# Kernel tuning notes

Hardware: AMD Instinct MI355X
Metric: run time of the kernel (lower is better)

## Reference

```python
import jax, jax.numpy as jnp
import numpy as np

EPS = 1e-6
N_HEADS, N_POINTS = 6, 4


def layer_norm(x, w, b):
    m = jnp.mean(x, -1, keepdims=True)
    v = jnp.mean((x - m) ** 2, -1, keepdims=True)
    return (x - m) * jax.lax.rsqrt(v + EPS) * w + b


def bilinear_sample(val, loc, Hl, Wl):
    # val: (B, nH, Hl*Wl, d); loc: (B, Lq, nH, P, 2) in [0,1]
    # matches F.grid_sample(mode='bilinear', padding='zeros', align_corners=False)
    B, nH, _, d = val.shape
    Lq, P = loc.shape[1], loc.shape[3]
    x = loc[..., 0] * Wl - 0.5
    y = loc[..., 1] * Hl - 0.5
    x0 = jnp.floor(x)
    y0 = jnp.floor(y)
    wx1 = x - x0
    wy1 = y - y0
    out = jnp.zeros((B, nH, Lq * P, d), val.dtype)
    corners = ((0, 0, (1 - wy1) * (1 - wx1)), (0, 1, (1 - wy1) * wx1),
               (1, 0, wy1 * (1 - wx1)), (1, 1, wy1 * wx1))
    for dy, dx, w in corners:
        xi = x0 + dx
        yi = y0 + dy
        valid = (xi >= 0) & (xi < Wl) & (yi >= 0) & (yi < Hl)
        xi_c = jnp.clip(xi, 0, Wl - 1).astype(jnp.int32)
        yi_c = jnp.clip(yi, 0, Hl - 1).astype(jnp.int32)
        idx = (yi_c * Wl + xi_c).transpose(0, 2, 1, 3).reshape(B, nH, Lq * P)
        g = jnp.take_along_axis(val, idx[..., None], axis=2)  # (B,nH,Lq*P,d)
        ww = jnp.where(valid, w, 0.0).transpose(0, 2, 1, 3).reshape(B, nH, Lq * P)
        out = out + g * ww[..., None]
    return out.reshape(B, nH, Lq, P, d).transpose(0, 2, 1, 3, 4)  # (B,Lq,nH,P,d)


def dwconv3x3(x, w, b):
    # x: (N, C, H, W); w: (C, 1, 3, 3) depthwise
    y = jax.lax.conv_general_dilated(x, w, (1, 1), 'SAME',
                                     feature_group_count=w.shape[0],
                                     dimension_numbers=('NCHW', 'OIHW', 'NCHW'))
    return y + b[None, :, None, None]


def setup_inputs() -> dict:
    key = jax.random.key(0)
    ks = jax.random.split(key, 16)
    B, H, W, C = 8, 32, 32, 768
    Lq = 3 * H * W
    Hf = Wf = 64
    hidden = int(C * 0.25)
    s = 0.02
    inp = {
        'query': jax.random.normal(ks[0], (B, Lq, C), jnp.float32),
        'reference_points': jax.random.uniform(ks[1], (B, Lq, 1, 2), jnp.float32),
        'feat': jax.random.normal(ks[2], (B, Hf * Wf, C), jnp.float32),
        'spatial_shapes': jnp.array([[Hf, Wf]], jnp.int32),
        'level_start_index': jnp.zeros((1,), jnp.int32),
        'H': H, 'W': W,
        'qn_w': jnp.ones((C,)), 'qn_b': jnp.zeros((C,)),
        'fn_w': jnp.ones((C,)), 'fn_b': jnp.zeros((C,)),
        'so_w': jax.random.normal(ks[3], (C, N_HEADS * N_POINTS * 2)) * s,
        'so_b': jax.random.normal(ks[4], (N_HEADS * N_POINTS * 2,)) * s,
        'aw_w': jax.random.normal(ks[5], (C, N_HEADS * N_POINTS)) * s,
        'aw_b': jnp.zeros((N_HEADS * N_POINTS,)),
        'vp_w': jax.random.normal(ks[6], (C, C)) * s,
        'vp_b': jnp.zeros((C,)),
        'op_w': jax.random.normal(ks[7], (C, C)) * s,
        'op_b': jnp.zeros((C,)),
        'ffn_w': jnp.ones((C,)), 'ffn_b': jnp.zeros((C,)),
        'fc1_w': jax.random.normal(ks[8], (C, hidden)) * s,
        'fc1_b': jnp.zeros((hidden,)),
        'dw_w': jax.random.normal(ks[9], (hidden, 1, 3, 3)) * s,
        'dw_b': jnp.zeros((hidden,)),
        'fc2_w': jax.random.normal(ks[10], (hidden, C)) * s,
        'fc2_b': jnp.zeros((C,)),
    }
    return inp


def reference(query, reference_points, feat, spatial_shapes, level_start_index, H, W,
              qn_w, qn_b, fn_w, fn_b, so_w, so_b, aw_w, aw_b, vp_w, vp_b, op_w, op_b,
              ffn_w, ffn_b, fc1_w, fc1_b, dw_w, dw_b, fc2_w, fc2_b):
    B, Lq, C = query.shape
    nH, nP = N_HEADS, N_POINTS
    d = C // nH
    ss = np.asarray(spatial_shapes)
    Hl, Wl = int(ss[0, 0]), int(ss[0, 1])

    # --- MSDeformAttn (single level) ---
    q = layer_norm(query, qn_w, qn_b)
    f = layer_norm(feat, fn_w, fn_b)
    value = (f @ vp_w + vp_b).reshape(B, Hl * Wl, nH, d).transpose(0, 2, 1, 3)  # (B,nH,Lin,d)
    offs = (q @ so_w + so_b).reshape(B, Lq, nH, 1, nP, 2)
    aw = jax.nn.softmax((q @ aw_w + aw_b).reshape(B, Lq, nH, nP), axis=-1)
    normalizer = jnp.array([Wl, Hl], query.dtype)
    loc = reference_points[:, :, None, :, None, :] + offs / normalizer  # (B,Lq,nH,1,nP,2)
    sampled = bilinear_sample(value, loc[:, :, :, 0], Hl, Wl)           # (B,Lq,nH,nP,d)
    attn = (sampled * aw[..., None]).sum(3).reshape(B, Lq, C) @ op_w + op_b
    query = query + attn

    # --- ConvFFN (3 equal HxW chunks through shared depthwise conv) ---
    x = layer_norm(query, ffn_w, ffn_b) @ fc1_w + fc1_b  # (B, 3*H*W, hid)
    n = Lq // 3
    hid = fc1_w.shape[1]
    xc = x.reshape(B, 3, n, hid).transpose(0, 1, 3, 2).reshape(B * 3, hid, H, W)
    xc = dwconv3x3(xc, dw_w, dw_b)
    x = xc.reshape(B, 3, hid, n).transpose(0, 1, 3, 2).reshape(B, Lq, hid)
    x = jax.nn.gelu(x, approximate=False)
    x = x @ fc2_w + fc2_b
    return query + x
```

## Files before the change

### kernel.cpp

```cpp
#include <hip/hip_runtime.h>
#include <hip/hip_bf16.h>
#include <math.h>

typedef __hip_bfloat16 bf16;
typedef short bf16x8 __attribute__((ext_vector_type(8)));
typedef short bf16x4 __attribute__((ext_vector_type(4)));
typedef float f32x4 __attribute__((ext_vector_type(4)));

#define NB 8
#define LQ 3072
#define CC 768
#define NHEADS 6
#define NPTS 4
#define DHEAD 128
#define HLVL 64
#define WLVL 64
#define LIN 4096
#define HID 192
#define BLTOT 24576
#define FROWS 32768

__device__ __forceinline__ float bf2f(short u)
{ return __uint_as_float(((unsigned)(unsigned short)u) << 16); }

template<int N_>
__device__ __forceinline__ void wait_vmcnt()
{
    if constexpr (N_ == 0)      asm volatile("s_waitcnt vmcnt(0)" ::: "memory");
    else if constexpr (N_ == 2) asm volatile("s_waitcnt vmcnt(2)" ::: "memory");
    else if constexpr (N_ == 4) asm volatile("s_waitcnt vmcnt(4)" ::: "memory");
    else if constexpr (N_ == 6) asm volatile("s_waitcnt vmcnt(6)" ::: "memory");
    else if constexpr (N_ == 8) asm volatile("s_waitcnt vmcnt(8)" ::: "memory");
    else static_assert(N_ == 0, "add a vmcnt case");
}

__global__ __launch_bounds__(256)
void ln_f32_wave_kernel(const float* __restrict__ x, const float* __restrict__ w,
                        const float* __restrict__ b, bf16* __restrict__ out)
{
    const int row = blockIdx.x * 4 + (threadIdx.x >> 6);
    const int lane = threadIdx.x & 63;
    const f32x4* xr = (const f32x4*)(x + (size_t)row * CC);
    f32x4 f0 = xr[lane], f1 = xr[64 + lane], f2 = xr[128 + lane];
    float s = 0.f, ss = 0.f;
    #pragma unroll
    for (int k = 0; k < 4; ++k) {
        s += f0[k] + f1[k] + f2[k];
        ss += f0[k] * f0[k] + f1[k] * f1[k] + f2[k] * f2[k];
    }
    #pragma unroll
    for (int o = 32; o > 0; o >>= 1) { s += __shfl_down(s, o); ss += __shfl_down(ss, o); }
    s = __shfl(s, 0); ss = __shfl(ss, 0);
    const float m = s * (1.f / CC);
    const float rs = rsqrtf(ss * (1.f / CC) - m * m + 1e-6f);
    const f32x4* w4 = (const f32x4*)w;
    const f32x4* b4 = (const f32x4*)b;
    bf16* orow = out + (size_t)row * CC;
    #pragma unroll
    for (int j = 0; j < 3; ++j) {
        f32x4 fj = (j == 0) ? f0 : (j == 1) ? f1 : f2;
        f32x4 wj = w4[j * 64 + lane], bj = b4[j * 64 + lane];
        bf16 t4[4];
        #pragma unroll
        for (int k = 0; k < 4; ++k) t4[k] = __float2bfloat16((fj[k] - m) * rs * wj[k] + bj[k]);
        *(bf16x4*)(orow + j * 256 + lane * 4) = *(bf16x4*)t4;
    }
}

__global__ __launch_bounds__(256)
void wt_bf16_kernel(const float* __restrict__ src, bf16* __restrict__ dst, int K, int N)
{
    __shared__ float t[64][65];
    const int tn0 = blockIdx.x * 64, tk0 = blockIdx.y * 64;
    const int r = threadIdx.x >> 6, c = threadIdx.x & 63;
    #pragma unroll
    for (int i = 0; i < 16; ++i) {
        const int k = i * 4 + r;
        t[k][c] = src[(size_t)(tk0 + k) * N + tn0 + c];
    }
    __syncthreads();
    #pragma unroll
    for (int i = 0; i < 16; ++i) {
        const int n = i * 4 + r;
        dst[(size_t)(tn0 + n) * K + tk0 + c] = __float2bfloat16(t[c][n]);
    }
}

__global__ __launch_bounds__(256)
void build_dots_w(const float* __restrict__ so_w, const float* __restrict__ so_b,
                  const float* __restrict__ aw_w, const float* __restrict__ aw_b,
                  bf16* __restrict__ wt, float* __restrict__ db)
{
    int i = blockIdx.x * 256 + threadIdx.x;
    if (i < 128 * 768) {
        int n = i / 768, k = i - n * 768;
        float v = 0.f;
        if (n < 48) v = so_w[(size_t)k * 48 + n];
        else if (n < 72) v = aw_w[(size_t)k * 24 + (n - 48)];
        wt[i] = __float2bfloat16(v);
    }
    if (i < 128) {
        float bv = 0.f;
        if (i < 48) bv = so_b[i];
        else if (i < 72) bv = aw_b[i - 48];
        db[i] = bv;
    }
}

template<int BM, int BN, int WM, int WN, int MODE>
__global__ __launch_bounds__(256)
void gemm_kernel(const bf16* __restrict__ A, const bf16* __restrict__ Bt,
                 const float* __restrict__ bias, const void* __restrict__ resv,
                 void* __restrict__ outv, int M, int N, int K)
{
    constexpr int WAVES_N = BN / WN;
    constexpr int FM = WM / 16, FN = WN / 16;
    constexpr int CWA = BM / 32;
    constexpr int CWB = BN / 32;
    constexpr int LPT = CWA + CWB;
    constexpr int ABYTES = BM * 256;
    constexpr int DBUF_BYTES = (BM + BN) * 256;
    constexpr int EPI_BYTES = BM * BN * 4;
    constexpr size_t SMEM_BYTES = DBUF_BYTES > EPI_BYTES ? DBUF_BYTES : EPI_BYTES;
    __shared__ __align__(16) char smem[SMEM_BYTES];
    bf16* sA = (bf16*)smem;
    bf16* sB = (bf16*)(smem + ABYTES);
    float* epi = (float*)smem;

    const int tid = threadIdx.x;
    const int lane = tid & 63;
    const int wave = tid >> 6;

    const int nwgx = gridDim.x;
    const int nwg = nwgx * gridDim.y;
    const int bid = blockIdx.y * nwgx + blockIdx.x;
    const int swz = (bid & 7) * (nwg >> 3) + (bid >> 3);
    const int m0 = (swz / nwgx) * BM;
    const int n0 = (swz % nwgx) * BN;

    const int wm = (wave / WAVES_N) * WM;
    const int wn = (wave % WAVES_N) * WN;

    const int srow = lane >> 3;
    const int scol = ((lane & 7) ^ srow) * 8;

    constexpr int GPR8 = BN / 8;
    constexpr int GPT8 = (BM * BN / 8) / 256;
    constexpr int QPR4 = BN / 4;
    constexpr int QPT4 = (BM * BN / 4) / 256;
    float4 pr0[GPT8], pr1[GPT8];
    bf16x4 prb[QPT4];
    if constexpr (MODE == 3) {
        const float* resf = (const float*)resv;
        #pragma unroll
        for (int k = 0; k < GPT8; ++k) {
            const int f = k * 256 + tid;
            const int rr = f / GPR8, cc = (f % GPR8) * 8;
            const size_t gidx = (size_t)(m0 + rr) * N + n0 + cc;
            pr0[k] = *(const float4*)&resf[gidx];
            pr1[k] = *(const float4*)&resf[gidx + 4];
        }
    }
    if constexpr (MODE == 4) {
        const bf16* resb = (const bf16*)resv;
        #pragma unroll
        for (int k = 0; k < QPT4; ++k) {
            const int f = k * 256 + tid;
            const int rr = f / QPR4, cc = (f % QPR4) * 4;
            prb[k] = *(const bf16x4*)&resb[(size_t)(m0 + rr) * N + n0 + cc];
        }
    }

#define STAGE(tt, half)                                                                            \
    { const int k0_ = (tt) * 64;                                                                   \
      _Pragma("unroll")                                                                            \
      for (int i_ = 0; i_ < CWA; ++i_) {                                                           \
        const int c_ = i_ * 4 + wave;                                                              \
        __builtin_amdgcn_global_load_lds(                                                          \
          (const __attribute__((address_space(1))) void*)(A + (size_t)(m0 + c_ * 8 + srow) * K + k0_ + scol), \
          (__attribute__((address_space(3))) void*)(sA + (half) * (BM * 64) + c_ * 512), 16, 0, 0); } \
      _Pragma("unroll")                                                                            \
      for (int i_ = 0; i_ < CWB; ++i_) {                                                           \
        const int c_ = i_ * 4 + wave;                                                              \
        __builtin_amdgcn_global_load_lds(                                                          \
          (const __attribute__((address_space(1))) void*)(Bt + (size_t)(n0 + c_ * 8 + srow) * K + k0_ + scol), \
          (__attribute__((address_space(3))) void*)(sB + (half) * (BN * 64) + c_ * 512), 16, 0, 0); } }

    f32x4 acc[FM][FN] = {};
    const int nt = K >> 6;

    STAGE(0, 0);
    STAGE(1, 1);

    for (int t = 0; t < nt; ++t) {
        const int half = t & 1;
        if (t + 1 < nt) wait_vmcnt<LPT>();
        else            wait_vmcnt<0>();
        __builtin_amdgcn_s_barrier();
        const bf16* cA = sA + half * (BM * 64);
        const bf16* cB = sB + half * (BN * 64);
        #pragma unroll
        for (int kki = 0; kki < 2; ++kki) {
            const int kslot = kki * 4 + (lane >> 4);
            bf16x8 aF[FM], bF[FN];
            #pragma unroll
            for (int i = 0; i < FM; ++i) {
                const int row = wm + i * 16 + (lane & 15);
                aF[i] = *(const bf16x8*)(&cA[row * 64 + ((kslot ^ (row & 7)) * 8)]);
            }
            #pragma unroll
            for (int j = 0; j < FN; ++j) {
                const int row = wn + j * 16 + (lane & 15);
                bF[j] = *(const bf16x8*)(&cB[row * 64 + ((kslot ^ (row & 7)) * 8)]);
            }
            #pragma unroll
            for (int i = 0; i < FM; ++i) {
                #pragma unroll
                for (int j = 0; j < FN; ++j)
                    acc[i][j] = __builtin_amdgcn_mfma_f32_16x16x32_bf16(aF[i], bF[j], acc[i][j], 0, 0, 0);
            }
        }
        asm volatile("s_waitcnt lgkmcnt(0)" ::: "memory");
        __builtin_amdgcn_s_barrier();
        if (t + 2 < nt) STAGE(t + 2, half);
    }
#undef STAGE

    #pragma unroll
    for (int j = 0; j < FN; ++j) {
        const int colL = wn + j * 16 + (lane & 15);
        const float bj = bias[n0 + colL];
        #pragma unroll
        for (int i = 0; i < FM; ++i) {
            #pragma unroll
            for (int r = 0; r < 4; ++r) {
                const int rowL = wm + i * 16 + ((lane >> 4) << 2) + r;
                const int addr = rowL * BN + ((((colL >> 2) ^ (rowL & 7)) << 2) | (colL & 3));
                epi[addr] = acc[i][j][r] + bj;
            }
        }
    }
    __syncthreads();

    if constexpr (MODE == 0 || MODE == 3) {
        #pragma unroll
        for (int k = 0; k < GPT8; ++k) {
            const int f = k * 256 + tid;
            const int rr = f / GPR8, cc = (f % GPR8) * 8;
            const int g0 = ((cc >> 2) ^ (rr & 7)) << 2;
            const int g1 = (((cc >> 2) + 1) ^ (rr & 7)) << 2;
            float4 v0 = *(const float4*)&epi[rr * BN + g0];
            float4 v1 = *(const float4*)&epi[rr * BN + g1];
            if constexpr (MODE == 3) {
                v0.x += pr0[k].x; v0.y += pr0[k].y; v0.z += pr0[k].z; v0.w += pr0[k].w;
                v1.x += pr1[k].x; v1.y += pr1[k].y; v1.z += pr1[k].z; v1.w += pr1[k].w;
            }
            bf16 tmp[8];
            tmp[0] = __float2bfloat16(v0.x); tmp[1] = __float2bfloat16(v0.y);
            tmp[2] = __float2bfloat16(v0.z); tmp[3] = __float2bfloat16(v0.w);
            tmp[4] = __float2bfloat16(v1.x); tmp[5] = __float2bfloat16(v1.y);
            tmp[6] = __float2bfloat16(v1.z); tmp[7] = __float2bfloat16(v1.w);
            *(bf16x8*)((bf16*)outv + (size_t)(m0 + rr) * N + n0 + cc) = *(bf16x8*)tmp;
        }
    } else {
        #pragma unroll
        for (int k = 0; k < QPT4; ++k) {
            const int f = k * 256 + tid;
            const int rr = f / QPR4, cc = (f % QPR4) * 4;
            const int gs = ((cc >> 2) ^ (rr & 7)) << 2;
            float4 v = *(const float4*)&epi[rr * BN + gs];
            if constexpr (MODE == 4) {
                v.x += bf2f(prb[k][0]); v.y += bf2f(prb[k][1]);
                v.z += bf2f(prb[k][2]); v.w += bf2f(prb[k][3]);
            }
            *(float4*)&((float*)outv)[(size_t)(m0 + rr) * N + n0 + cc] = v;
        }
    }
}

template<int BM, int BN, int WM, int WN, bool F32IN, int EPI>
__global__ __launch_bounds__(256)
void ln_gemm_kernel(const void* __restrict__ xv, const float* __restrict__ lnw,
                    const float* __restrict__ lnb, const bf16* __restrict__ Bt,
                    const float* __restrict__ bias, const float* __restrict__ refp,
                    void* __restrict__ outv, int M, int N)
{
    constexpr int WAVES_N = BN / WN;
    constexpr int FM = WM / 16, FN = WN / 16;
    constexpr int CWB = BN / 32;
    constexpr int RPW = BM / 4;
    static_assert(BM * BN * 4 <= 2 * BN * 64 * 2, "epi must fit in sB");
    __shared__ __align__(16) bf16 sA[BM * 768];
    __shared__ __align__(16) char sBmem[2 * BN * 64 * 2];
    bf16* sB = (bf16*)sBmem;
    float* epi = (float*)sBmem;

    const int tid = threadIdx.x;
    const int lane = tid & 63;
    const int wave = tid >> 6;

    const int nwgx = gridDim.x;
    const int nwg = nwgx * gridDim.y;
    const int bid = blockIdx.y * nwgx + blockIdx.x;
    const int swz = (bid & 7) * (nwg >> 3) + (bid >> 3);
    const int m0 = (swz / nwgx) * BM;
    const int n0 = (swz % nwgx) * BN;

    const int wm = (wave / WAVES_N) * WM;
    const int wn = (wave % WAVES_N) * WN;
    const int srow = lane >> 3;
    const int scol = ((lane & 7) ^ srow) * 8;

#define STAGEB(tt, half)                                                                           \
    { const int k0_ = (tt) * 64;                                                                   \
      _Pragma("unroll")                                                                            \
      for (int i_ = 0; i_ < CWB; ++i_) {                                                           \
        const int c_ = i_ * 4 + wave;                                                              \
        __builtin_amdgcn_global_load_lds(                                                          \
          (const __attribute__((address_space(1))) void*)(Bt + (size_t)(n0 + c_ * 8 + srow) * 768 + k0_ + scol), \
          (__attribute__((address_space(3))) void*)(sB + (half) * (BN * 64) + c_ * 512), 16, 0, 0); } }

    STAGEB(0, 0);
    STAGEB(1, 1);

    if constexpr (F32IN) {
        const f32x4* w4 = (const f32x4*)lnw;
        const f32x4* b4 = (const f32x4*)lnb;
        f32x4 wv0 = w4[lane], wv1 = w4[64 + lane], wv2 = w4[128 + lane];
        f32x4 bv0 = b4[lane], bv1 = b4[64 + lane], bv2 = b4[128 + lane];
        for (int rr = 0; rr < RPW; ++rr) {
            const int r = wave * RPW + rr;
            const f32x4* xr = (const f32x4*)((const float*)xv + (size_t)(m0 + r) * 768);
            f32x4 f0 = xr[lane], f1 = xr[64 + lane], f2 = xr[128 + lane];
            float s = 0.f, ss = 0.f;
            #pragma unroll
            for (int k = 0; k < 4; ++k) {
                s += f0[k] + f1[k] + f2[k];
                ss += f0[k] * f0[k] + f1[k] * f1[k] + f2[k] * f2[k];
            }
            #pragma unroll
            for (int o = 32; o > 0; o >>= 1) { s += __shfl_down(s, o); ss += __shfl_down(ss, o); }
            s = __shfl(s, 0); ss = __shfl(ss, 0);
            const float mn = s * (1.f / 768);
            const float rs = rsqrtf(ss * (1.f / 768) - mn * mn + 1e-6f);
            const int rx7 = r & 7;
            const int slot = (lane >> 1) & 7;
            const int off = (lane & 1) * 4;
            #pragma unroll
            for (int j = 0; j < 3; ++j) {
                f32x4 fj = (j == 0) ? f0 : (j == 1) ? f1 : f2;
                f32x4 wj = (j == 0) ? wv0 : (j == 1) ? wv1 : wv2;
                f32x4 bj = (j == 0) ? bv0 : (j == 1) ? bv1 : bv2;
                bf16 t4[4];
                #pragma unroll
                for (int k = 0; k < 4; ++k)
                    t4[k] = __float2bfloat16((fj[k] - mn) * rs * wj[k] + bj[k]);
                const int kt = j * 4 + (lane >> 4);
                *(bf16x4*)&sA[r * 768 + kt * 64 + ((slot ^ rx7) << 3) + off] = *(bf16x4*)t4;
            }
        }
    } else {
        const f32x4* w4 = (const f32x4*)lnw;
        const f32x4* b4 = (const f32x4*)lnb;
        f32x4 w80 = w4[lane * 2], w81 = w4[lane * 2 + 1], w44 = w4[128 + lane];
        f32x4 b80 = b4[lane * 2], b81 = b4[lane * 2 + 1], b44 = b4[128 + lane];
        for (int rr = 0; rr < RPW; ++rr) {
            const int r = wave * RPW + rr;
            const bf16* xr = (const bf16*)xv + (size_t)(m0 + r) * 768;
            bf16x8 v8 = *(const bf16x8*)(xr + lane * 8);
            bf16x4 v4 = *(const bf16x4*)(xr + 512 + lane * 4);
            float f[12];
            #pragma unroll
            for (int k = 0; k < 8; ++k) f[k] = bf2f(v8[k]);
            #pragma unroll
            for (int k = 0; k < 4; ++k) f[8 + k] = bf2f(v4[k]);
            float s = 0.f, ss = 0.f;
            #pragma unroll
            for (int k = 0; k < 12; ++k) { s += f[k]; ss += f[k] * f[k]; }
            #pragma unroll
            for (int o = 32; o > 0; o >>= 1) { s += __shfl_down(s, o); ss += __shfl_down(ss, o); }
            s = __shfl(s, 0); ss = __shfl(ss, 0);
            const float mn = s * (1.f / 768);
            const float rs = rsqrtf(ss * (1.f / 768) - mn * mn + 1e-6f);
            const int rx7 = r & 7;
            bf16 t8[8];
            #pragma unroll
            for (int k = 0; k < 4; ++k) t8[k] = __float2bfloat16((f[k] - mn) * rs * w80[k] + b80[k]);
            #pragma unroll
            for (int k = 0; k < 4; ++k) t8[4 + k] = __float2bfloat16((f[4 + k] - mn) * rs * w81[k] + b81[k]);
            *(bf16x8*)&sA[r * 768 + (lane >> 3) * 64 + (((lane & 7) ^ rx7) << 3)] = *(bf16x8*)t8;
            bf16 t4[4];
            #pragma unroll
            for (int k = 0; k < 4; ++k) t4[k] = __float2bfloat16((f[8 + k] - mn) * rs * w44[k] + b44[k]);
            *(bf16x4*)&sA[r * 768 + (8 + (lane >> 4)) * 64 + ((((lane >> 1) & 7) ^ rx7) << 3) + (lane & 1) * 4]
                = *(bf16x4*)t4;
        }
    }
    asm volatile("s_waitcnt lgkmcnt(0)" ::: "memory");

    f32x4 acc[FM][FN] = {};
    for (int t = 0; t < 12; ++t) {
        const int half = t & 1;
        if (t + 1 < 12) wait_vmcnt<CWB>();
        else            wait_vmcnt<0>();
        __builtin_amdgcn_s_barrier();
        const bf16* cB = sB + half * (BN * 64);
        #pragma unroll
        for (int kki = 0; kki < 2; ++kki) {
            const int kslot = kki * 4 + (lane >> 4);
            bf16x8 aF[FM], bF[FN];
            #pragma unroll
            for (int i = 0; i < FM; ++i) {
                const int row = wm + i * 16 + (lane & 15);
                aF[i] = *(const bf16x8*)(&sA[row * 768 + t * 64 + ((kslot ^ (row & 7)) * 8)]);
            }
            #pragma unroll
            for (int j = 0; j < FN; ++j) {
                const int row = wn + j * 16 + (lane & 15);
                bF[j] = *(const bf16x8*)(&cB[row * 64 + ((kslot ^ (row & 7)) * 8)]);
            }
            #pragma unroll
            for (int i = 0; i < FM; ++i) {
                #pragma unroll
                for (int j = 0; j < FN; ++j)
                    acc[i][j] = __builtin_amdgcn_mfma_f32_16x16x32_bf16(aF[i], bF[j], acc[i][j], 0, 0, 0);
            }
        }
        asm volatile("s_waitcnt lgkmcnt(0)" ::: "memory");
        __builtin_amdgcn_s_barrier();
        if (t + 2 < 12) STAGEB(t + 2, half);
    }
#undef STAGEB

    #pragma unroll
    for (int j = 0; j < FN; ++j) {
        const int colL = wn + j * 16 + (lane & 15);
        const float bj = bias[n0 + colL];
        #pragma unroll
        for (int i = 0; i < FM; ++i) {
            #pragma unroll
            for (int r = 0; r < 4; ++r) {
                const int rowL = wm + i * 16 + ((lane >> 4) << 2) + r;
                const int addr = rowL * BN + ((((colL >> 2) ^ (rowL & 7)) << 2) | (colL & 3));
                epi[addr] = acc[i][j][r] + bj;
            }
        }
    }
    __syncthreads();

    if constexpr (EPI == 1) {
        if (tid < BM * NHEADS) {
            const int rowL = tid & (BM - 1);
            const int h = tid / BM;
            auto erd = [&](int col) -> float {
                return epi[rowL * BN + ((((col >> 2) ^ (rowL & 7)) << 2) | (col & 3))];
            };
            float l0 = erd(48 + h * 4 + 0), l1 = erd(48 + h * 4 + 1);
            float l2 = erd(48 + h * 4 + 2), l3 = erd(48 + h * 4 + 3);
            float mx = fmaxf(fmaxf(l0, l1), fmaxf(l2, l3));
            float e0 = expf(l0 - mx), e1 = expf(l1 - mx), e2 = expf(l2 - mx), e3 = expf(l3 - mx);
            float inv = 1.f / (e0 + e1 + e2 + e3);
            float ee[4] = {e0, e1, e2, e3};
            const float rx = refp[(size_t)(m0 + rowL) * 2];
            const float ry = refp[(size_t)(m0 + rowL) * 2 + 1];
            float4* pp = (float4*)outv + ((size_t)(m0 + rowL) * NHEADS + h) * 4;
            #pragma unroll
            for (int p = 0; p < 4; ++p) {
                float ox = erd(h * 8 + p * 2), oy = erd(h * 8 + p * 2 + 1);
                pp[p] = make_float4(rx + ox * (1.f / WLVL), ry + oy * (1.f / HLVL), ee[p] * inv, 0.f);
            }
        }
    } else {
        constexpr int GPR8 = BN / 8;
        constexpr int GPT8 = (BM * BN / 8) / 256;
        #pragma unroll
        for (int k = 0; k < GPT8; ++k) {
            const int f = k * 256 + tid;
            const int rr = f / GPR8, cc = (f % GPR8) * 8;
            const int g0 = ((cc >> 2) ^ (rr & 7)) << 2;
            const int g1 = (((cc >> 2) + 1) ^ (rr & 7)) << 2;
            float4 v0 = *(const float4*)&epi[rr * BN + g0];
            float4 v1 = *(const float4*)&epi[rr * BN + g1];
            bf16 tmp[8];
            tmp[0] = __float2bfloat16(v0.x); tmp[1] = __float2bfloat16(v0.y);
            tmp[2] = __float2bfloat16(v0.z); tmp[3] = __float2bfloat16(v0.w);
            tmp[4] = __float2bfloat16(v1.x); tmp[5] = __float2bfloat16(v1.y);
            tmp[6] = __float2bfloat16(v1.z); tmp[7] = __float2bfloat16(v1.w);
            *(bf16x8*)((bf16*)outv + (size_t)(m0 + rr) * N + n0 + cc) = *(bf16x8*)tmp;
        }
    }
}

__global__ __launch_bounds__(256)
void sampler_kernel(const bf16* __restrict__ value, const float4* __restrict__ params,
                    bf16* __restrict__ attn_in)
{
    const int tid = threadIdx.x;
    const int cpx = gridDim.x >> 3;
    const int gblk = (blockIdx.x & 7) * cpx + (blockIdx.x >> 3);
    const int g = gblk * 16 + (tid >> 4);
    const int lane16 = tid & 15;
    const int bl = g / NHEADS;
    const int h = g - bl * NHEADS;
    const int b = bl / LQ;
    const bf16* vh = value + (size_t)b * LIN * CC + h * DHEAD + lane16 * 8;

    int offs[16];
    float wgt[16];
    #pragma unroll
    for (int p = 0; p < NPTS; ++p) {
        float4 pr = params[(size_t)g * 4 + p];
        float x = pr.x * (float)WLVL - 0.5f;
        float y = pr.y * (float)HLVL - 0.5f;
        float x0f = floorf(x), y0f = floorf(y);
        float wx1 = x - x0f, wy1 = y - y0f;
        float wx0 = 1.f - wx1, wy0 = 1.f - wy1;
        int x0 = (int)x0f, y0 = (int)y0f;
        #pragma unroll
        for (int dy = 0; dy < 2; ++dy) {
            const int yi = y0 + dy;
            const int yc = min(max(yi, 0), HLVL - 1);
            const float wy = (dy ? wy1 : wy0) * ((yi >= 0 && yi < HLVL) ? pr.z : 0.f);
            #pragma unroll
            for (int dx = 0; dx < 2; ++dx) {
                const int xi = x0 + dx;
                const int xc = min(max(xi, 0), WLVL - 1);
                const int idx = p * 4 + dy * 2 + dx;
                offs[idx] = (yc * WLVL + xc) * CC;
                wgt[idx] = wy * (dx ? wx1 : wx0) * ((xi >= 0 && xi < WLVL) ? 1.f : 0.f);
            }
        }
    }
    bf16x8 v[16];
    #pragma unroll
    for (int i = 0; i < 16; ++i) v[i] = *(const bf16x8*)(vh + offs[i]);
    float acc[8] = {};
    #pragma unroll
    for (int i = 0; i < 16; ++i) {
        #pragma unroll
        for (int j = 0; j < 8; ++j)
            acc[j] += wgt[i] * bf2f(v[i][j]);
    }
    bf16 tmp[8];
    #pragma unroll
    for (int j = 0; j < 8; ++j) tmp[j] = __float2bfloat16(acc[j]);
    *(bf16x8*)(attn_in + (size_t)bl * CC + h * DHEAD + lane16 * 8) = *(bf16x8*)tmp;
}

__global__ __launch_bounds__(192)
void dwconv_gelu_kernel(const bf16* __restrict__ z, const float* __restrict__ dw_w,
                        const float* __restrict__ dw_b, bf16* __restrict__ g)
{
    const int tp = threadIdx.x / 48;
    const int tc = threadIdx.x % 48;
    const int m = blockIdx.x * 4 + tp;
    const int c = tc * 4;
    const int pix = m & 1023;
    const int h = pix >> 5, w = pix & 31;
    float acc[4];
    #pragma unroll
    for (int j = 0; j < 4; ++j) acc[j] = dw_b[c + j];
    #pragma unroll
    for (int dy = -1; dy <= 1; ++dy) {
        int hh2 = h + dy;
        if (hh2 < 0 || hh2 >= 32) continue;
        #pragma unroll
        for (int dx = -1; dx <= 1; ++dx) {
            int ww2 = w + dx;
            if (ww2 < 0 || ww2 >= 32) continue;
            bf16x4 vv = *(const bf16x4*)&z[(size_t)(m + dy * 32 + dx) * HID + c];
            #pragma unroll
            for (int j = 0; j < 4; ++j)
                acc[j] += bf2f(vv[j]) * dw_w[(c + j) * 9 + (dy + 1) * 3 + (dx + 1)];
        }
    }
    bf16 tmp[4];
    #pragma unroll
    for (int j = 0; j < 4; ++j) {
        float ge = acc[j] * 0.5f * (1.f + erff(acc[j] * 0.70710678118f));
        tmp[j] = __float2bfloat16(ge);
    }
    *(bf16x4*)&g[(size_t)m * HID + c] = *(bf16x4*)tmp;
}

extern "C" void kernel_launch(void* const* d_in, const int* in_sizes, int n_in,
                              void* d_out, int out_size, void* d_ws, size_t ws_size,
                              hipStream_t stream)
{
    const float* query = (const float*)d_in[0];
    const float* refp  = (const float*)d_in[1];
    const float* feat  = (const float*)d_in[2];
    const float* qn_w = (const float*)d_in[7];
    const float* qn_b = (const float*)d_in[8];
    const float* fn_w = (const float*)d_in[9];
    const float* fn_b = (const float*)d_in[10];
    const float* so_w = (const float*)d_in[11];
    const float* so_b = (const float*)d_in[12];
    const float* aw_w = (const float*)d_in[13];
    const float* aw_b = (const float*)d_in[14];
    const float* vp_w = (const float*)d_in[15];
    const float* vp_b = (const float*)d_in[16];
    const float* op_w = (const float*)d_in[17];
    const float* op_b = (const float*)d_in[18];
    const float* ffn_w = (const float*)d_in[19];
    const float* ffn_b = (const float*)d_in[20];
    const float* fc1_w = (const float*)d_in[21];
    const float* fc1_b = (const float*)d_in[22];
    const float* dw_w = (const float*)d_in[23];
    const float* dw_b = (const float*)d_in[24];
    const float* fc2_w = (const float*)d_in[25];
    const float* fc2_b = (const float*)d_in[26];
    float* out = (float*)d_out;

    if (ws_size < (size_t)125829632) return;
    char* ws = (char*)d_ws;
    bf16* vp_wt   = (bf16*)(ws + 0);
    bf16* op_wt   = (bf16*)(ws + 1179648);
    bf16* fc1_wt  = (bf16*)(ws + 2359296);
    bf16* fc2_wt  = (bf16*)(ws + 2654208);
    bf16* dots_wt = (bf16*)(ws + 2949120);
    float* dots_b = (float*)(ws + 3145728);
    char* paramsR = ws + 3146240;
    char* dotsR   = ws + 12583424;
    char* regA = ws + 25166336;
    char* regB = ws + 75497984;
    float4* params = (float4*)paramsR;
    bf16* g        = (bf16*)paramsR;
    bf16* z        = (bf16*)dotsR;
    bf16* f_ln    = (bf16*)regA;
    bf16* attn_in = (bf16*)regA;
    bf16* value = (bf16*)regB;
    bf16* s_bf  = (bf16*)regB;

    wt_bf16_kernel<<<dim3(12, 12), 256, 0, stream>>>(vp_w, vp_wt, 768, 768);
    wt_bf16_kernel<<<dim3(12, 12), 256, 0, stream>>>(op_w, op_wt, 768, 768);
    wt_bf16_kernel<<<dim3(3, 12), 256, 0, stream>>>(fc1_w, fc1_wt, 768, 192);
    wt_bf16_kernel<<<dim3(12, 3), 256, 0, stream>>>(fc2_w, fc2_wt, 192, 768);
    build_dots_w<<<384, 256, 0, stream>>>(so_w, so_b, aw_w, aw_b, dots_wt, dots_b);

    ln_gemm_kernel<32, 128, 16, 64, true, 1><<<dim3(1, BLTOT / 32), 256, 0, stream>>>(
        query, qn_w, qn_b, dots_wt, dots_b, refp, params, BLTOT, 128);
    ln_f32_wave_kernel<<<FROWS / 4, 256, 0, stream>>>(feat, fn_w, fn_b, f_ln);
    gemm_kernel<128, 128, 64, 64, 0><<<dim3(6, FROWS / 128), 256, 0, stream>>>(
        f_ln, vp_wt, vp_b, nullptr, value, FROWS, 768, 768);
    sampler_kernel<<<(BLTOT * NHEADS) / 16, 256, 0, stream>>>(value, params, attn_in);
    gemm_kernel<64, 128, 32, 64, 3><<<dim3(6, BLTOT / 64), 256, 0, stream>>>(
        attn_in, op_wt, op_b, query, s_bf, BLTOT, 768, 768);

    ln_gemm_kernel<32, 64, 32, 16, false, 0><<<dim3(3, BLTOT / 32), 256, 0, stream>>>(
        s_bf, ffn_w, ffn_b, fc1_wt, fc1_b, nullptr, z, BLTOT, HID);
    dwconv_gelu_kernel<<<BLTOT / 4, 192, 0, stream>>>(z, dw_w, dw_b, g);
    gemm_kernel<64, 128, 32, 64, 4><<<dim3(6, BLTOT / 64), 256, 0, stream>>>(
        g, fc2_wt, fc2_b, s_bf, out, BLTOT, 768, HID);
}
```

Baseline: 327.2 us.

## Triple-buffer GEMM K-tiles and merge weight-prep launches into one kernel

Both GEMM kernels move from double to triple buffering of the K-tile shared memory stages, issuing loads three tiles ahead with matching vmcnt waits, so global-to-LDS latency is hidden more deeply. The five small weight transpose/convert launches are merged into a single prep kernel dispatched by block index, removing per-launch overhead. The extra buffer raises LDS use per block, which may lower occupancy, especially in ln_gemm where sA is already large.

```diff
diff --git a/kernel.cpp b/kernel.cpp
--- a/kernel.cpp
+++ b/kernel.cpp
@@ -26,11 +26,13 @@
 template<int N_>
 __device__ __forceinline__ void wait_vmcnt()
 {
-    if constexpr (N_ == 0)      asm volatile("s_waitcnt vmcnt(0)" ::: "memory");
-    else if constexpr (N_ == 2) asm volatile("s_waitcnt vmcnt(2)" ::: "memory");
-    else if constexpr (N_ == 4) asm volatile("s_waitcnt vmcnt(4)" ::: "memory");
-    else if constexpr (N_ == 6) asm volatile("s_waitcnt vmcnt(6)" ::: "memory");
-    else if constexpr (N_ == 8) asm volatile("s_waitcnt vmcnt(8)" ::: "memory");
+    if constexpr (N_ == 0)       asm volatile("s_waitcnt vmcnt(0)" ::: "memory");
+    else if constexpr (N_ == 2)  asm volatile("s_waitcnt vmcnt(2)" ::: "memory");
+    else if constexpr (N_ == 4)  asm volatile("s_waitcnt vmcnt(4)" ::: "memory");
+    else if constexpr (N_ == 6)  asm volatile("s_waitcnt vmcnt(6)" ::: "memory");
+    else if constexpr (N_ == 8)  asm volatile("s_waitcnt vmcnt(8)" ::: "memory");
+    else if constexpr (N_ == 12) asm volatile("s_waitcnt vmcnt(12)" ::: "memory");
+    else if constexpr (N_ == 16) asm volatile("s_waitcnt vmcnt(16)" ::: "memory");
     else static_assert(N_ == 0, "add a vmcnt case");
 }
 
@@ -67,43 +69,50 @@
     }
 }
 
+__device__ __forceinline__ void wt_tile(float (*t)[65], const float* __restrict__ src,
+                                        bf16* __restrict__ dst, int K, int N, int tn0, int tk0)
+{
+    const int r = threadIdx.x >> 6, c = threadIdx.x & 63;
+    #pragma unroll
+    for (int i = 0; i < 16; ++i)
+        t[i * 4 + r][c] = src[(size_t)(tk0 + i * 4 + r) * N + tn0 + c];
+    __syncthreads();
+    #pragma unroll
+    for (int i = 0; i < 16; ++i)
+        dst[(size_t)(tn0 + i * 4 + r) * K + tk0 + c] = __float2bfloat16(t[c][i * 4 + r]);
+}
+
 __global__ __launch_bounds__(256)
-void wt_bf16_kernel(const float* __restrict__ src, bf16* __restrict__ dst, int K, int N)
+void prep_kernel(const float* __restrict__ vp_w, const float* __restrict__ op_w,
+                 const float* __restrict__ fc1_w, const float* __restrict__ fc2_w,
+                 const float* __restrict__ so_w, const float* __restrict__ so_b,
+                 const float* __restrict__ aw_w, const float* __restrict__ aw_b,
+                 bf16* __restrict__ vp_wt, bf16* __restrict__ op_wt,
+                 bf16* __restrict__ fc1_wt, bf16* __restrict__ fc2_wt,
+                 bf16* __restrict__ dots_wt, float* __restrict__ db)
 {
     __shared__ float t[64][65];
-    const int tn0 = blockIdx.x * 64, tk0 = blockIdx.y * 64;
-    const int r = threadIdx.x >> 6, c = threadIdx.x & 63;
-    #pragma unroll
-    for (int i = 0; i < 16; ++i) {
-        const int k = i * 4 + r;
-        t[k][c] = src[(size_t)(tk0 + k) * N + tn0 + c];
-    }
-    __syncthreads();
-    #pragma unroll
-    for (int i = 0; i < 16; ++i) {
-        const int n = i * 4 + r;
-        dst[(size_t)(tn0 + n) * K + tk0 + c] = __float2bfloat16(t[c][n]);
-    }
-}
-
-__global__ __launch_bounds__(256)
-void build_dots_w(const float* __restrict__ so_w, const float* __restrict__ so_b,
-                  const float* __restrict__ aw_w, const float* __restrict__ aw_b,
-                  bf16* __restrict__ wt, float* __restrict__ db)
-{
-    int i = blockIdx.x * 256 + threadIdx.x;
-    if (i < 128 * 768) {
-        int n = i / 768, k = i - n * 768;
-        float v = 0.f;
-        if (n < 48) v = so_w[(size_t)k * 48 + n];
-        else if (n < 72) v = aw_w[(size_t)k * 24 + (n - 48)];
-        wt[i] = __float2bfloat16(v);
-    }
-    if (i < 128) {
-        float bv = 0.f;
-        if (i < 48) bv = so_b[i];
-        else if (i < 72) bv = aw_b[i - 48];
-        db[i] = bv;
+    int b = blockIdx.x;
+    if (b < 144)      wt_tile(t, vp_w, vp_wt, 768, 768, (b % 12) * 64, (b / 12) * 64);
+    else if (b < 288) { b -= 144; wt_tile(t, op_w, op_wt, 768, 768, (b % 12) * 64, (b / 12) * 64); }
+    else if (b < 324) { b -= 288; wt_tile(t, fc1_w, fc1_wt, 768, 192, (b % 3) * 64, (b / 3) * 64); }
+    else if (b < 360) { b -= 324; wt_tile(t, fc2_w, fc2_wt, 192, 768, (b % 12) * 64, (b / 12) * 64); }
+    else {
+        b -= 360;
+        int i = b * 256 + threadIdx.x;
+        if (i < 128 * 768) {
+            int n = i / 768, k = i - n * 768;
+            float v = 0.f;
+            if (n < 48) v = so_w[(size_t)k * 48 + n];
+            else if (n < 72) v = aw_w[(size_t)k * 24 + (n - 48)];
+            dots_wt[i] = __float2bfloat16(v);
+        }
+        if (i < 128) {
+            float bv = 0.f;
+            if (i < 48) bv = so_b[i];
+            else if (i < 72) bv = aw_b[i - 48];
+            db[i] = bv;
+        }
     }
 }
 
@@ -118,8 +127,8 @@
     constexpr int CWA = BM / 32;
     constexpr int CWB = BN / 32;
     constexpr int LPT = CWA + CWB;
-    constexpr int ABYTES = BM * 256;
-    constexpr int DBUF_BYTES = (BM + BN) * 256;
+    constexpr int ABYTES = 3 * BM * 128;
+    constexpr int DBUF_BYTES = 3 * (BM + BN) * 128;
     constexpr int EPI_BYTES = BM * BN * 4;
     constexpr size_t SMEM_BYTES = DBUF_BYTES > EPI_BYTES ? DBUF_BYTES : EPI_BYTES;
     __shared__ __align__(16) char smem[SMEM_BYTES];
@@ -171,34 +180,36 @@
         }
     }
 
-#define STAGE(tt, half)                                                                            \
+#define STAGE(tt, buf)                                                                             \
     { const int k0_ = (tt) * 64;                                                                   \
       _Pragma("unroll")                                                                            \
       for (int i_ = 0; i_ < CWA; ++i_) {                                                           \
         const int c_ = i_ * 4 + wave;                                                              \
         __builtin_amdgcn_global_load_lds(                                                          \
           (const __attribute__((address_space(1))) void*)(A + (size_t)(m0 + c_ * 8 + srow) * K + k0_ + scol), \
-          (__attribute__((address_space(3))) void*)(sA + (half) * (BM * 64) + c_ * 512), 16, 0, 0); } \
+          (__attribute__((address_space(3))) void*)(sA + (buf) * (BM * 64) + c_ * 512), 16, 0, 0); } \
       _Pragma("unroll")                                                                            \
       for (int i_ = 0; i_ < CWB; ++i_) {                                                           \
         const int c_ = i_ * 4 + wave;                                                              \
         __builtin_amdgcn_global_load_lds(                                                          \
           (const __attribute__((address_space(1))) void*)(Bt + (size_t)(n0 + c_ * 8 + srow) * K + k0_ + scol), \
-          (__attribute__((address_space(3))) void*)(sB + (half) * (BN * 64) + c_ * 512), 16, 0, 0); } }
+          (__attribute__((address_space(3))) void*)(sB + (buf) * (BN * 64) + c_ * 512), 16, 0, 0); } }
 
     f32x4 acc[FM][FN] = {};
     const int nt = K >> 6;
 
     STAGE(0, 0);
     STAGE(1, 1);
-
+    STAGE(2, 2);
+
+    int buf = 0;
     for (int t = 0; t < nt; ++t) {
-        const int half = t & 1;
-        if (t + 1 < nt) wait_vmcnt<LPT>();
-        else            wait_vmcnt<0>();
+        if (t + 2 < nt)      wait_vmcnt<2 * LPT>();
+        else if (t + 1 < nt) wait_vmcnt<LPT>();
+        else                 wait_vmcnt<0>();
         __builtin_amdgcn_s_barrier();
-        const bf16* cA = sA + half * (BM * 64);
-        const bf16* cB = sB + half * (BN * 64);
+        const bf16* cA = sA + buf * (BM * 64);
+        const bf16* cB = sB + buf * (BN * 64);
         #pragma unroll
         for (int kki = 0; kki < 2; ++kki) {
             const int kslot = kki * 4 + (lane >> 4);
@@ -222,7 +233,8 @@
         }
         asm volatile("s_waitcnt lgkmcnt(0)" ::: "memory");
         __builtin_amdgcn_s_barrier();
-        if (t + 2 < nt) STAGE(t + 2, half);
+        if (t + 3 < nt) STAGE(t + 3, buf);
+        buf = (buf == 2) ? 0 : buf + 1;
     }
 #undef STAGE
 
@@ -289,9 +301,9 @@
     constexpr int FM = WM / 16, FN = WN / 16;
     constexpr int CWB = BN / 32;
     constexpr int RPW = BM / 4;
-    static_assert(BM * BN * 4 <= 2 * BN * 64 * 2, "epi must fit in sB");
+    static_assert(BM * BN * 4 <= 3 * BN * 64 * 2, "epi must fit in sB");
     __shared__ __align__(16) bf16 sA[BM * 768];
-    __shared__ __align__(16) char sBmem[2 * BN * 64 * 2];
+    __shared__ __align__(16) char sBmem[3 * BN * 64 * 2];
     bf16* sB = (bf16*)sBmem;
     float* epi = (float*)sBmem;
 
@@ -311,17 +323,18 @@
     const int srow = lane >> 3;
     const int scol = ((lane & 7) ^ srow) * 8;
 
-#define STAGEB(tt, half)                                                                           \
+#define STAGEB(tt, buf)                                                                            \
     { const int k0_ = (tt) * 64;                                                                   \
       _Pragma("unroll")                                                                            \
       for (int i_ = 0; i_ < CWB; ++i_) {                                                           \
         const int c_ = i_ * 4 + wave;                                                              \
         __builtin_amdgcn_global_load_lds(                                                          \
           (const __attribute__((address_space(1))) void*)(Bt + (size_t)(n0 + c_ * 8 + srow) * 768 + k0_ + scol), \
-          (__attribute__((address_space(3))) void*)(sB + (half) * (BN * 64) + c_ * 512), 16, 0, 0); } }
+          (__attribute__((address_space(3))) void*)(sB + (buf) * (BN * 64) + c_ * 512), 16, 0, 0); } }
 
     STAGEB(0, 0);
     STAGEB(1, 1);
+    STAGEB(2, 2);
 
     if constexpr (F32IN) {
         const f32x4* w4 = (const f32x4*)lnw;
@@ -399,12 +412,14 @@
     asm volatile("s_waitcnt lgkmcnt(0)" ::: "memory");
 
     f32x4 acc[FM][FN] = {};
+    #pragma unroll
     for (int t = 0; t < 12; ++t) {
-        const int half = t & 1;
-        if (t + 1 < 12) wait_vmcnt<CWB>();
-        else            wait_vmcnt<0>();
+        const int buf = t % 3;
+        if (t + 2 < 12)      wait_vmcnt<2 * CWB>();
+        else if (t + 1 < 12) wait_vmcnt<CWB>();
+        else                 wait_vmcnt<0>();
         __builtin_amdgcn_s_barrier();
-        const bf16* cB = sB + half * (BN * 64);
+        const bf16* cB = sB + buf * (BN * 64);
         #pragma unroll
         for (int kki = 0; kki < 2; ++kki) {
             const int kslot = kki * 4 + (lane >> 4);
@@ -428,7 +443,7 @@
         }
         asm volatile("s_waitcnt lgkmcnt(0)" ::: "memory");
         __builtin_amdgcn_s_barrier();
-        if (t + 2 < 12) STAGEB(t + 2, half);
+        if (t + 3 < 12) STAGEB(t + 3, buf);
     }
 #undef STAGEB
 
@@ -632,11 +647,8 @@
     bf16* value = (bf16*)regB;
     bf16* s_bf  = (bf16*)regB;
 
-    wt_bf16_kernel<<<dim3(12, 12), 256, 0, stream>>>(vp_w, vp_wt, 768, 768);
-    wt_bf16_kernel<<<dim3(12, 12), 256, 0, stream>>>(op_w, op_wt, 768, 768);
-    wt_bf16_kernel<<<dim3(3, 12), 256, 0, stream>>>(fc1_w, fc1_wt, 768, 192);
-    wt_bf16_kernel<<<dim3(12, 3), 256, 0, stream>>>(fc2_w, fc2_wt, 192, 768);
-    build_dots_w<<<384, 256, 0, stream>>>(so_w, so_b, aw_w, aw_b, dots_wt, dots_b);
+    prep_kernel<<<744, 256, 0, stream>>>(vp_w, op_w, fc1_w, fc2_w, so_w, so_b, aw_w, aw_b,
+                                         vp_wt, op_wt, fc1_wt, fc2_wt, dots_wt, dots_b);
 
     ln_gemm_kernel<32, 128, 16, 64, true, 1><<<dim3(1, BLTOT / 32), 256, 0, stream>>>(
         query, qn_w, qn_b, dots_wt, dots_b, refp, params, BLTOT, 128);
```

After: 345.8 us. 5.7% more time.
